# Optimization experiments

Hardware: AMD Instinct MI355X
Metric: run time of the kernel (lower is better)

The kernel has to match this reference:

```python
import jax, jax.numpy as jnp
import numpy as np

Z_FAR = 1000.0
LAST_DIST = 1e10


def setup_inputs() -> dict:
    key = jax.random.key(0)
    ks = jax.random.split(key, 5)
    B, H, W, P, F = 1, 128, 128, 128, 64
    HW = H * W
    return {
        "sigma": jax.random.normal(ks[0], (B, HW, P), dtype=jnp.float32),
        "feat": jax.random.normal(ks[1], (B, HW, P, F), dtype=jnp.float32),
        "depth": jax.random.uniform(ks[2], (B, HW, P), dtype=jnp.float32),
        "semantic": jax.random.normal(ks[3], (B, HW, P), dtype=jnp.float32),
        "rays_dir": jax.random.normal(ks[4], (B, HW, 3), dtype=jnp.float32),
        "H": H,
        "W": W,
    }


def _volume_weights(z_vals, ray_vector, sigma):
    # dists[i] = z[i+1]-z[i], last dist = LAST_DIST, scaled by |ray|
    dists = jnp.concatenate(
        [z_vals[..., 1:] - z_vals[..., :-1],
         jnp.full_like(z_vals[..., :1], LAST_DIST)], axis=-1)
    dists = dists * jnp.linalg.norm(ray_vector, axis=-1, keepdims=True)
    alpha = 1.0 - jnp.exp(-jax.nn.relu(sigma) * dists)
    trans = jnp.cumprod(
        jnp.concatenate([jnp.ones_like(alpha[..., :1]), 1.0 - alpha + 1e-10],
                        axis=-1), axis=-1)[..., :-1]
    return alpha * trans


def reference(sigma, feat, depth, semantic, rays_dir, H, W):
    B = depth.shape[0]
    # sort_samples: sort every field along the sample axis by depth
    idx = jnp.argsort(depth, axis=-1)                       # [B, HW, P]
    depth_s = jnp.take_along_axis(depth, idx, axis=-1)
    sigma_s = jnp.take_along_axis(sigma, idx, axis=-1)
    semantic_s = jnp.take_along_axis(semantic, idx, axis=-1)
    feat_s = jnp.take_along_axis(feat, idx[..., None], axis=-2)

    weights = _volume_weights(depth_s, rays_dir, sigma_s)   # [B, HW, P]
    feat_map = jnp.sum(weights[..., None] * feat_s, axis=-2)  # [B, HW, F]

    # L1-normalized weights for depth (torch F.normalize p=1, eps=1e-12)
    wd = weights / jnp.maximum(
        jnp.sum(jnp.abs(weights), axis=-1, keepdims=True), 1e-12)
    depth_map = jnp.sum(wd * depth_s, axis=-1, keepdims=True)  # [B, HW, 1]
    depth_map = jnp.clip((depth_map - 0.001) / (Z_FAR - 0.001), 0.0, 1.0)

    depth_map = depth_map.transpose(0, 2, 1).reshape(B, -1, H, W)
    feat_map = feat_map.transpose(0, 2, 1).reshape(B, -1, H, W)
    alpha_map = jnp.sum(weights, axis=-1).reshape(B, 1, H, W)
    return feat_map, depth_map, alpha_map, weights
```

## Files before the change

### kernel.cpp

```cpp
#include <hip/hip_runtime.h>
#include <stdint.h>

#define HW 16384
#define P 128
#define F 64

#define WAVE_SYNC()                                          \
    do {                                                     \
        asm volatile("s_waitcnt lgkmcnt(0)" ::: "memory");   \
        __builtin_amdgcn_sched_barrier(0);                   \
    } while (0)

__global__ __launch_bounds__(256) void nerf_wave_kernel(
    const float* __restrict__ sigma,
    const float* __restrict__ feat,
    const float* __restrict__ depth,
    const float* __restrict__ rays_dir,
    float* __restrict__ out_feat,
    float* __restrict__ out_depth,
    float* __restrict__ out_alpha,
    float* __restrict__ out_weights)
{
    const int tid  = threadIdx.x;
    const int lane = tid & 63;
    const int wv   = tid >> 6;
    const int r    = blockIdx.x * 4 + wv;

    __shared__ float lsdep[4][P];
    __shared__ float lssig[4][P];
    __shared__ int   lplist[4][P];
    __shared__ float lswc[4][P];
    float* sdep  = lsdep[wv];
    float* ssig  = lssig[wv];
    int*   plist = lplist[wv];
    float* swc   = lswc[wv];

    const float d0 = depth[(size_t)r * P + lane];
    const float d1 = depth[(size_t)r * P + 64 + lane];
    const float g0 = sigma[(size_t)r * P + lane];
    const float g1 = sigma[(size_t)r * P + 64 + lane];
    const float rx = rays_dir[r * 3 + 0];
    const float ry = rays_dir[r * 3 + 1];
    const float rz = rays_dir[r * 3 + 2];
    const float rn = sqrtf(rx * rx + ry * ry + rz * rz);

    const unsigned b0 = __float_as_uint(d0);
    const unsigned b1 = __float_as_uint(d1);
    int rank0 = 0, rank1 = 0;
    #pragma unroll 8
    for (int j = 0; j < 64; ++j) {
        const unsigned q0 = (unsigned)__shfl((int)b0, j);
        const unsigned q1 = (unsigned)__shfl((int)b1, j);
        rank0 += (q0 < b0 || (q0 == b0 && j < lane)) ? 1 : 0;
        rank0 += (q1 < b0) ? 1 : 0;
        rank1 += (q0 < b1 || q0 == b1) ? 1 : 0;
        rank1 += (q1 < b1 || (q1 == b1 && j < lane)) ? 1 : 0;
    }

    sdep[rank0] = d0; sdep[rank1] = d1;
    ssig[rank0] = g0; ssig[rank1] = g1;
    WAVE_SYNC();
    const float sd_lo = sdep[lane];
    const float sd_hi = sdep[64 + lane];
    const float sg_lo = ssig[lane];
    const float sg_hi = ssig[64 + lane];

    float dn_lo = __shfl_down(sd_lo, 1);
    const float sd_hi0 = __shfl(sd_hi, 0);
    if (lane == 63) dn_lo = sd_hi0;
    const float dn_hi = __shfl_down(sd_hi, 1);
    const float dz_lo = dn_lo - sd_lo;
    const float dz_hi = (lane == 63) ? 1e10f : (dn_hi - sd_hi);

    const float a_lo  = 1.0f - expf(-fmaxf(sg_lo, 0.0f) * dz_lo * rn);
    const float a_hi  = 1.0f - expf(-fmaxf(sg_hi, 0.0f) * dz_hi * rn);
    const float tp_lo = (1.0f - a_lo) + 1e-10f;
    const float tp_hi = (1.0f - a_hi) + 1e-10f;

    float sc_lo = tp_lo, sc_hi = tp_hi;
    #pragma unroll
    for (int off = 1; off < 64; off <<= 1) {
        const float vl = __shfl_up(sc_lo, off);
        const float vh = __shfl_up(sc_hi, off);
        if (lane >= off) { sc_lo *= vl; sc_hi *= vh; }
    }
    const float tot_lo = __shfl(sc_lo, 63);
    float tr_lo = __shfl_up(sc_lo, 1);
    float tr_hi = __shfl_up(sc_hi, 1);
    if (lane == 0) { tr_lo = 1.0f; tr_hi = 1.0f; }
    tr_hi *= tot_lo;
    const float w_lo = a_lo * tr_lo;
    const float w_hi = a_hi * tr_hi;

    out_weights[(size_t)r * P + lane]      = w_lo;
    out_weights[(size_t)r * P + 64 + lane] = w_hi;

    float s1 = w_lo + w_hi;
    float s2 = w_lo * sd_lo + w_hi * sd_hi;
    #pragma unroll
    for (int off = 32; off > 0; off >>= 1) {
        s1 += __shfl_xor(s1, off);
        s2 += __shfl_xor(s2, off);
    }
    if (lane == 0) {
        float dm = s2 / fmaxf(s1, 1e-12f);
        dm = (dm - 0.001f) / (1000.0f - 0.001f);
        dm = fminf(fmaxf(dm, 0.0f), 1.0f);
        out_depth[r] = dm;
        out_alpha[r] = s1;
    }

    const float wa0 = __shfl(w_lo, rank0 & 63);
    const float wb0 = __shfl(w_hi, rank0 & 63);
    const float wo0 = (rank0 < 64) ? wa0 : wb0;
    const float wa1 = __shfl(w_lo, rank1 & 63);
    const float wb1 = __shfl(w_hi, rank1 & 63);
    const float wo1 = (rank1 < 64) ? wa1 : wb1;

    const unsigned long long m0 = __ballot(wo0 != 0.0f);
    const unsigned long long m1 = __ballot(wo1 != 0.0f);
    const int M = (int)(__popcll(m0) + __popcll(m1));
    const unsigned long long lmask = (1ull << lane) - 1ull;
    if (wo0 != 0.0f) {
        const int pos = (int)__popcll(m0 & lmask);
        plist[pos] = lane; swc[pos] = wo0;
    }
    if (wo1 != 0.0f) {
        const int pos = (int)__popcll(m0) + (int)__popcll(m1 & lmask);
        plist[pos] = 64 + lane; swc[pos] = wo1;
    }
    WAVE_SYNC();

    const int f4   = lane & 15;
    const int psub = lane >> 4;
    const float4* fp = (const float4*)(feat + (size_t)r * P * F);
    const int jcap = (M > 0) ? (M - 1) : 0;
    const int nch  = (M + 31) >> 5;

    float4 acc = make_float4(0.f, 0.f, 0.f, 0.f);
    for (int c = 0; c < nch; ++c) {
        const int base = c * 32;
        int   pj[8];
        float wj[8];
        #pragma unroll
        for (int i = 0; i < 8; ++i) {
            const int idx = base + i * 4 + psub;
            const int j   = (idx < M) ? idx : jcap;
            pj[i] = plist[j] & (P - 1);
            wj[i] = (idx < M) ? swc[j] : 0.0f;
        }
        float4 fv[8];
        #pragma unroll
        for (int i = 0; i < 8; ++i)
            fv[i] = fp[pj[i] * (F / 4) + f4];
        #pragma unroll
        for (int i = 0; i < 8; ++i) {
            acc.x += wj[i] * fv[i].x;
            acc.y += wj[i] * fv[i].y;
            acc.z += wj[i] * fv[i].z;
            acc.w += wj[i] * fv[i].w;
        }
    }

    acc.x += __shfl_xor(acc.x, 16); acc.y += __shfl_xor(acc.y, 16);
    acc.z += __shfl_xor(acc.z, 16); acc.w += __shfl_xor(acc.w, 16);
    acc.x += __shfl_xor(acc.x, 32); acc.y += __shfl_xor(acc.y, 32);
    acc.z += __shfl_xor(acc.z, 32); acc.w += __shfl_xor(acc.w, 32);

    if (psub == 0) {
        const int f = f4 * 4;
        out_feat[(size_t)(f + 0) * HW + r] = acc.x;
        out_feat[(size_t)(f + 1) * HW + r] = acc.y;
        out_feat[(size_t)(f + 2) * HW + r] = acc.z;
        out_feat[(size_t)(f + 3) * HW + r] = acc.w;
    }
}

extern "C" void kernel_launch(void* const* d_in, const int* in_sizes, int n_in,
                              void* d_out, int out_size, void* d_ws, size_t ws_size,
                              hipStream_t stream) {
    const float* sigma    = (const float*)d_in[0];
    const float* feat     = (const float*)d_in[1];
    const float* depth    = (const float*)d_in[2];
    const float* rays_dir = (const float*)d_in[4];

    float* out = (float*)d_out;
    float* out_feat    = out;
    float* out_depth   = out + (size_t)F * HW;
    float* out_alpha   = out_depth + HW;
    float* out_weights = out_alpha + HW;

    nerf_wave_kernel<<<HW / 4, 256, 0, stream>>>(sigma, feat, depth, rays_dir,
                                                 out_feat, out_depth, out_alpha,
                                                 out_weights);
}
```

Before: 59.26 us.

## Process 16 rays per block and stage feature outputs in LDS for coalesced stores

```diff
diff --git a/kernel.cpp b/kernel.cpp
--- a/kernel.cpp
+++ b/kernel.cpp
@@ -21,159 +21,177 @@
     float* __restrict__ out_alpha,
     float* __restrict__ out_weights)
 {
-    const int tid  = threadIdx.x;
-    const int lane = tid & 63;
-    const int wv   = tid >> 6;
-    const int r    = blockIdx.x * 4 + wv;
+    const int tid   = threadIdx.x;
+    const int lane  = tid & 63;
+    const int wv    = tid >> 6;
+    const int rbase = blockIdx.x * 16;
 
     __shared__ float lsdep[4][P];
     __shared__ float lssig[4][P];
     __shared__ int   lplist[4][P];
     __shared__ float lswc[4][P];
+    __shared__ float stile[F][17];
+    __shared__ float sdm[16];
+    __shared__ float sam[16];
     float* sdep  = lsdep[wv];
     float* ssig  = lssig[wv];
     int*   plist = lplist[wv];
     float* swc   = lswc[wv];
 
-    const float d0 = depth[(size_t)r * P + lane];
-    const float d1 = depth[(size_t)r * P + 64 + lane];
-    const float g0 = sigma[(size_t)r * P + lane];
-    const float g1 = sigma[(size_t)r * P + 64 + lane];
-    const float rx = rays_dir[r * 3 + 0];
-    const float ry = rays_dir[r * 3 + 1];
-    const float rz = rays_dir[r * 3 + 2];
-    const float rn = sqrtf(rx * rx + ry * ry + rz * rz);
-
-    const unsigned b0 = __float_as_uint(d0);
-    const unsigned b1 = __float_as_uint(d1);
-    int rank0 = 0, rank1 = 0;
-    #pragma unroll 8
-    for (int j = 0; j < 64; ++j) {
-        const unsigned q0 = (unsigned)__shfl((int)b0, j);
-        const unsigned q1 = (unsigned)__shfl((int)b1, j);
-        rank0 += (q0 < b0 || (q0 == b0 && j < lane)) ? 1 : 0;
-        rank0 += (q1 < b0) ? 1 : 0;
-        rank1 += (q0 < b1 || q0 == b1) ? 1 : 0;
-        rank1 += (q1 < b1 || (q1 == b1 && j < lane)) ? 1 : 0;
-    }
-
-    sdep[rank0] = d0; sdep[rank1] = d1;
-    ssig[rank0] = g0; ssig[rank1] = g1;
-    WAVE_SYNC();
-    const float sd_lo = sdep[lane];
-    const float sd_hi = sdep[64 + lane];
-    const float sg_lo = ssig[lane];
-    const float sg_hi = ssig[64 + lane];
-
-    float dn_lo = __shfl_down(sd_lo, 1);
-    const float sd_hi0 = __shfl(sd_hi, 0);
-    if (lane == 63) dn_lo = sd_hi0;
-    const float dn_hi = __shfl_down(sd_hi, 1);
-    const float dz_lo = dn_lo - sd_lo;
-    const float dz_hi = (lane == 63) ? 1e10f : (dn_hi - sd_hi);
-
-    const float a_lo  = 1.0f - expf(-fmaxf(sg_lo, 0.0f) * dz_lo * rn);
-    const float a_hi  = 1.0f - expf(-fmaxf(sg_hi, 0.0f) * dz_hi * rn);
-    const float tp_lo = (1.0f - a_lo) + 1e-10f;
-    const float tp_hi = (1.0f - a_hi) + 1e-10f;
-
-    float sc_lo = tp_lo, sc_hi = tp_hi;
-    #pragma unroll
-    for (int off = 1; off < 64; off <<= 1) {
-        const float vl = __shfl_up(sc_lo, off);
-        const float vh = __shfl_up(sc_hi, off);
-        if (lane >= off) { sc_lo *= vl; sc_hi *= vh; }
-    }
-    const float tot_lo = __shfl(sc_lo, 63);
-    float tr_lo = __shfl_up(sc_lo, 1);
-    float tr_hi = __shfl_up(sc_hi, 1);
-    if (lane == 0) { tr_lo = 1.0f; tr_hi = 1.0f; }
-    tr_hi *= tot_lo;
-    const float w_lo = a_lo * tr_lo;
-    const float w_hi = a_hi * tr_hi;
-
-    out_weights[(size_t)r * P + lane]      = w_lo;
-    out_weights[(size_t)r * P + 64 + lane] = w_hi;
-
-    float s1 = w_lo + w_hi;
-    float s2 = w_lo * sd_lo + w_hi * sd_hi;
-    #pragma unroll
-    for (int off = 32; off > 0; off >>= 1) {
-        s1 += __shfl_xor(s1, off);
-        s2 += __shfl_xor(s2, off);
-    }
-    if (lane == 0) {
-        float dm = s2 / fmaxf(s1, 1e-12f);
-        dm = (dm - 0.001f) / (1000.0f - 0.001f);
-        dm = fminf(fmaxf(dm, 0.0f), 1.0f);
-        out_depth[r] = dm;
-        out_alpha[r] = s1;
-    }
-
-    const float wa0 = __shfl(w_lo, rank0 & 63);
-    const float wb0 = __shfl(w_hi, rank0 & 63);
-    const float wo0 = (rank0 < 64) ? wa0 : wb0;
-    const float wa1 = __shfl(w_lo, rank1 & 63);
-    const float wb1 = __shfl(w_hi, rank1 & 63);
-    const float wo1 = (rank1 < 64) ? wa1 : wb1;
-
-    const unsigned long long m0 = __ballot(wo0 != 0.0f);
-    const unsigned long long m1 = __ballot(wo1 != 0.0f);
-    const int M = (int)(__popcll(m0) + __popcll(m1));
-    const unsigned long long lmask = (1ull << lane) - 1ull;
-    if (wo0 != 0.0f) {
-        const int pos = (int)__popcll(m0 & lmask);
-        plist[pos] = lane; swc[pos] = wo0;
-    }
-    if (wo1 != 0.0f) {
-        const int pos = (int)__popcll(m0) + (int)__popcll(m1 & lmask);
-        plist[pos] = 64 + lane; swc[pos] = wo1;
-    }
-    WAVE_SYNC();
-
     const int f4   = lane & 15;
     const int psub = lane >> 4;
-    const float4* fp = (const float4*)(feat + (size_t)r * P * F);
-    const int jcap = (M > 0) ? (M - 1) : 0;
-    const int nch  = (M + 31) >> 5;
-
-    float4 acc = make_float4(0.f, 0.f, 0.f, 0.f);
-    for (int c = 0; c < nch; ++c) {
-        const int base = c * 32;
-        int   pj[8];
-        float wj[8];
+
+    for (int i = 0; i < 4; ++i) {
+        const int r   = rbase + wv * 4 + i;
+        const int col = wv * 4 + i;
+
+        const float d0 = depth[(size_t)r * P + lane];
+        const float d1 = depth[(size_t)r * P + 64 + lane];
+        const float g0 = sigma[(size_t)r * P + lane];
+        const float g1 = sigma[(size_t)r * P + 64 + lane];
+        const float rx = rays_dir[r * 3 + 0];
+        const float ry = rays_dir[r * 3 + 1];
+        const float rz = rays_dir[r * 3 + 2];
+        const float rn = sqrtf(rx * rx + ry * ry + rz * rz);
+
+        const unsigned b0 = __float_as_uint(d0);
+        const unsigned b1 = __float_as_uint(d1);
+        int rank0 = 0, rank1 = 0;
+        #pragma unroll 8
+        for (int j = 0; j < 64; ++j) {
+            const unsigned q0 = (unsigned)__shfl((int)b0, j);
+            const unsigned q1 = (unsigned)__shfl((int)b1, j);
+            rank0 += (q0 < b0 || (q0 == b0 && j < lane)) ? 1 : 0;
+            rank0 += (q1 < b0) ? 1 : 0;
+            rank1 += (q0 < b1 || q0 == b1) ? 1 : 0;
+            rank1 += (q1 < b1 || (q1 == b1 && j < lane)) ? 1 : 0;
+        }
+
+        sdep[rank0] = d0; sdep[rank1] = d1;
+        ssig[rank0] = g0; ssig[rank1] = g1;
+        WAVE_SYNC();
+        const float sd_lo = sdep[lane];
+        const float sd_hi = sdep[64 + lane];
+        const float sg_lo = ssig[lane];
+        const float sg_hi = ssig[64 + lane];
+
+        float dn_lo = __shfl_down(sd_lo, 1);
+        const float sd_hi0 = __shfl(sd_hi, 0);
+        if (lane == 63) dn_lo = sd_hi0;
+        const float dn_hi = __shfl_down(sd_hi, 1);
+        const float dz_lo = dn_lo - sd_lo;
+        const float dz_hi = (lane == 63) ? 1e10f : (dn_hi - sd_hi);
+
+        const float a_lo  = 1.0f - expf(-fmaxf(sg_lo, 0.0f) * dz_lo * rn);
+        const float a_hi  = 1.0f - expf(-fmaxf(sg_hi, 0.0f) * dz_hi * rn);
+        const float tp_lo = (1.0f - a_lo) + 1e-10f;
+        const float tp_hi = (1.0f - a_hi) + 1e-10f;
+
+        float sc_lo = tp_lo, sc_hi = tp_hi;
         #pragma unroll
-        for (int i = 0; i < 8; ++i) {
-            const int idx = base + i * 4 + psub;
-            const int j   = (idx < M) ? idx : jcap;
-            pj[i] = plist[j] & (P - 1);
-            wj[i] = (idx < M) ? swc[j] : 0.0f;
-        }
-        float4 fv[8];
+        for (int off = 1; off < 64; off <<= 1) {
+            const float vl = __shfl_up(sc_lo, off);
+            const float vh = __shfl_up(sc_hi, off);
+            if (lane >= off) { sc_lo *= vl; sc_hi *= vh; }
+        }
+        const float tot_lo = __shfl(sc_lo, 63);
+        float tr_lo = __shfl_up(sc_lo, 1);
+        float tr_hi = __shfl_up(sc_hi, 1);
+        if (lane == 0) { tr_lo = 1.0f; tr_hi = 1.0f; }
+        tr_hi *= tot_lo;
+        const float w_lo = a_lo * tr_lo;
+        const float w_hi = a_hi * tr_hi;
+
+        out_weights[(size_t)r * P + lane]      = w_lo;
+        out_weights[(size_t)r * P + 64 + lane] = w_hi;
+
+        float s1 = w_lo + w_hi;
+        float s2 = w_lo * sd_lo + w_hi * sd_hi;
         #pragma unroll
-        for (int i = 0; i < 8; ++i)
-            fv[i] = fp[pj[i] * (F / 4) + f4];
-        #pragma unroll
-        for (int i = 0; i < 8; ++i) {
-            acc.x += wj[i] * fv[i].x;
-            acc.y += wj[i] * fv[i].y;
-            acc.z += wj[i] * fv[i].z;
-            acc.w += wj[i] * fv[i].w;
+        for (int off = 32; off > 0; off >>= 1) {
+            s1 += __shfl_xor(s1, off);
+            s2 += __shfl_xor(s2, off);
+        }
+        if (lane == 0) {
+            float dm = s2 / fmaxf(s1, 1e-12f);
+            dm = (dm - 0.001f) / (1000.0f - 0.001f);
+            dm = fminf(fmaxf(dm, 0.0f), 1.0f);
+            sdm[col] = dm;
+            sam[col] = s1;
+        }
+
+        const float wa0 = __shfl(w_lo, rank0 & 63);
+        const float wb0 = __shfl(w_hi, rank0 & 63);
+        const float wo0 = (rank0 < 64) ? wa0 : wb0;
+        const float wa1 = __shfl(w_lo, rank1 & 63);
+        const float wb1 = __shfl(w_hi, rank1 & 63);
+        const float wo1 = (rank1 < 64) ? wa1 : wb1;
+
+        const unsigned long long m0 = __ballot(wo0 != 0.0f);
+        const unsigned long long m1 = __ballot(wo1 != 0.0f);
+        const int M = (int)(__popcll(m0) + __popcll(m1));
+        const unsigned long long lmask = (1ull << lane) - 1ull;
+        if (wo0 != 0.0f) {
+            const int pos = (int)__popcll(m0 & lmask);
+            plist[pos] = lane; swc[pos] = wo0;
+        }
+        if (wo1 != 0.0f) {
+            const int pos = (int)__popcll(m0) + (int)__popcll(m1 & lmask);
+            plist[pos] = 64 + lane; swc[pos] = wo1;
+        }
+        WAVE_SYNC();
+
+        const float4* fp = (const float4*)(feat + (size_t)r * P * F);
+        const int jcap = (M > 0) ? (M - 1) : 0;
+        const int nch  = (M + 31) >> 5;
+
+        float4 acc = make_float4(0.f, 0.f, 0.f, 0.f);
+        for (int c = 0; c < nch; ++c) {
+            const int base = c * 32;
+            int   pj[8];
+            float wj[8];
+            #pragma unroll
+            for (int q = 0; q < 8; ++q) {
+                const int idx = base + q * 4 + psub;
+                const int j   = (idx < M) ? idx : jcap;
+                pj[q] = plist[j] & (P - 1);
+                wj[q] = (idx < M) ? swc[j] : 0.0f;
+            }
+            float4 fv[8];
+            #pragma unroll
+            for (int q = 0; q < 8; ++q)
+                fv[q] = fp[pj[q] * (F / 4) + f4];
+            #pragma unroll
+            for (int q = 0; q < 8; ++q) {
+                acc.x += wj[q] * fv[q].x;
+                acc.y += wj[q] * fv[q].y;
+                acc.z += wj[q] * fv[q].z;
+                acc.w += wj[q] * fv[q].w;
+            }
+        }
+
+        acc.x += __shfl_xor(acc.x, 16); acc.y += __shfl_xor(acc.y, 16);
+        acc.z += __shfl_xor(acc.z, 16); acc.w += __shfl_xor(acc.w, 16);
+        acc.x += __shfl_xor(acc.x, 32); acc.y += __shfl_xor(acc.y, 32);
+        acc.z += __shfl_xor(acc.z, 32); acc.w += __shfl_xor(acc.w, 32);
+
+        if (psub == 0) {
+            stile[f4 * 4 + 0][col] = acc.x;
+            stile[f4 * 4 + 1][col] = acc.y;
+            stile[f4 * 4 + 2][col] = acc.z;
+            stile[f4 * 4 + 3][col] = acc.w;
         }
     }
 
-    acc.x += __shfl_xor(acc.x, 16); acc.y += __shfl_xor(acc.y, 16);
-    acc.z += __shfl_xor(acc.z, 16); acc.w += __shfl_xor(acc.w, 16);
-    acc.x += __shfl_xor(acc.x, 32); acc.y += __shfl_xor(acc.y, 32);
-    acc.z += __shfl_xor(acc.z, 32); acc.w += __shfl_xor(acc.w, 32);
-
-    if (psub == 0) {
-        const int f = f4 * 4;
-        out_feat[(size_t)(f + 0) * HW + r] = acc.x;
-        out_feat[(size_t)(f + 1) * HW + r] = acc.y;
-        out_feat[(size_t)(f + 2) * HW + r] = acc.z;
-        out_feat[(size_t)(f + 3) * HW + r] = acc.w;
-    }
+    __syncthreads();
+
+    const int c  = tid & 15;
+    const int fr = tid >> 4;
+    #pragma unroll
+    for (int k = 0; k < 4; ++k)
+        out_feat[(size_t)(fr * 4 + k) * HW + rbase + c] = stile[fr * 4 + k][c];
+    if (tid < 16)      out_depth[rbase + tid] = sdm[tid];
+    else if (tid < 32) out_alpha[rbase + tid - 16] = sam[tid - 16];
 }
 
 extern "C" void kernel_launch(void* const* d_in, const int* in_sizes, int n_in,
@@ -190,7 +208,7 @@
     float* out_alpha   = out_depth + HW;
     float* out_weights = out_alpha + HW;
 
-    nerf_wave_kernel<<<HW / 4, 256, 0, stream>>>(sigma, feat, depth, rays_dir,
-                                                 out_feat, out_depth, out_alpha,
-                                                 out_weights);
+    nerf_wave_kernel<<<HW / 16, 256, 0, stream>>>(sigma, feat, depth, rays_dir,
+                                                  out_feat, out_depth, out_alpha,
+                                                  out_weights);
 }
```

Result: slower. 64.13 us (+8.2%).
